# Kernel optimization log

Measured on AMD Instinct MI355X. Metric: run time of the kernel, lower is better.

Reference implementation:

```python
import jax, jax.numpy as jnp
import numpy as np


def setup_inputs() -> dict:
    key = jax.random.key(0)
    ks = jax.random.split(key, 9)
    N, K, CS, CT, OUT, S = 50000, 16, 64, 64, 64, 4
    x = jax.random.normal(ks[0], (N, CT), dtype=jnp.float32)
    src = jax.random.normal(ks[1], (N, CS), dtype=jnp.float32)
    neighbor_idx = jax.random.randint(ks[2], (N, K), 0, N, dtype=jnp.int32)
    scale_t = 1.0 / np.sqrt(CT)
    scale_s = 1.0 / np.sqrt(CS)
    Wt = jax.random.normal(ks[3], (CT, S), dtype=jnp.float32) * scale_t
    bt = jax.random.normal(ks[4], (S,), dtype=jnp.float32) * scale_t
    Ws = jax.random.normal(ks[5], (CS, S), dtype=jnp.float32) * scale_s
    bs = jax.random.normal(ks[6], (S,), dtype=jnp.float32) * scale_s
    W_lin = jax.random.normal(ks[7], (S, CS, OUT), dtype=jnp.float32) * scale_s
    b_lin = jax.random.normal(ks[8], (S, OUT), dtype=jnp.float32) * scale_s
    return {"x": x, "src": src, "neighbor_idx": neighbor_idx,
            "Wt": Wt, "bt": bt, "Ws": Ws, "bs": bs,
            "W_lin": W_lin, "b_lin": b_lin}


def reference(x, src, neighbor_idx, Wt, bt, Ws, bs, W_lin, b_lin):
    # Gather per-node neighbor messages: [N, K, Cs]
    msgs = src[neighbor_idx]
    size = Wt.shape[-1]
    # target assignment logits from own data: [N, S]
    t = x @ Wt + bt
    # source assignment logits from messages: [N, K, S]
    s = jnp.einsum('nkc,cs->nks', msgs, Ws) + bs
    # soft assignment over the `size` weight matrices (softmax over S)
    a = jax.nn.softmax(s + t[:, None, :], axis=-1)  # [N, K, S]
    # apply each of the `size` linears to the messages: [N, K, S, O]
    w = jnp.einsum('nkc,sco->nkso', msgs, W_lin) + b_lin
    # assignment-weighted mean over the S weight matrices: [N, K, O]
    out = jnp.einsum('nks,nkso->nko', a, w) / size
    return out
```

## Files before the change

kernel.cpp:

```cpp
#include <hip/hip_runtime.h>

#define CT 64
#define CS 64
#define K_NB 16
#define S_SZ 4
#define OUT_C 64
#define CAP 64

typedef float vfloat4 __attribute__((ext_vector_type(4)));

__global__ __launch_bounds__(256) void kt_rowlin(
    const float* __restrict__ in, const float* __restrict__ W,
    const float* __restrict__ b, float* __restrict__ outp, int N)
{
    int gt = blockIdx.x * 256 + threadIdx.x;
    int r = gt >> 3, part = gt & 7;
    if (r >= N) return;
    const float4* rv = (const float4*)(in + (size_t)r * 64) + part * 2;
    const float4* W4 = (const float4*)W;
    float4 q0 = rv[0], q1 = rv[1];
    int c0 = part * 8;
    float4 acc = {0.f, 0.f, 0.f, 0.f};
    float xc[8] = {q0.x, q0.y, q0.z, q0.w, q1.x, q1.y, q1.z, q1.w};
    #pragma unroll
    for (int u = 0; u < 8; ++u) {
        float4 wv = W4[c0 + u];
        acc.x = fmaf(xc[u], wv.x, acc.x);
        acc.y = fmaf(xc[u], wv.y, acc.y);
        acc.z = fmaf(xc[u], wv.z, acc.z);
        acc.w = fmaf(xc[u], wv.w, acc.w);
    }
    #pragma unroll
    for (int m = 1; m < 8; m <<= 1) {
        acc.x += __shfl_xor(acc.x, m);
        acc.y += __shfl_xor(acc.y, m);
        acc.z += __shfl_xor(acc.z, m);
        acc.w += __shfl_xor(acc.w, m);
    }
    if (part == 0) {
        float4 bb = *(const float4*)b;
        acc.x += bb.x; acc.y += bb.y; acc.z += bb.z; acc.w += bb.w;
        ((float4*)outp)[r] = acc;
    }
}

__global__ __launch_bounds__(256) void kh_zero(int* __restrict__ cursor, int N)
{
    int i = blockIdx.x * 256 + threadIdx.x;
    if (i < N) cursor[i] = 0;
}

__global__ __launch_bounds__(256) void kh_fill_fixed(
    const int* __restrict__ nidx, int* __restrict__ cursor,
    int* __restrict__ plist, int NK)
{
    int p = blockIdx.x * 256 + threadIdx.x;
    if (p >= NK) return;
    int j = nidx[p];
    int pos = atomicAdd(&cursor[j], 1);
    if (pos < CAP) plist[(size_t)j * CAP + pos] = p;
}

__global__ __launch_bounds__(256) void k_main(
    const int* __restrict__ cursor, const int* __restrict__ plist,
    const float* __restrict__ src,
    const float* __restrict__ W_lin, const float* __restrict__ b_lin,
    const float* __restrict__ t_in, const float* __restrict__ sl_in,
    float* __restrict__ out, int N)
{
    const int col = threadIdx.x;
    const int s = col >> 6, o = col & 63;
    float w[64];
    #pragma unroll
    for (int c = 0; c < 64; ++c)
        w[c] = W_lin[s * 4096 + (c << 6) + o];
    const float bl = b_lin[col];
    const int g = col >> 4;
    const int lane16 = col & 15;
    __shared__ float4 lsrc4[2][16];
    __shared__ float4 zl4[2][64];

    const int stride = gridDim.x;
    int j = blockIdx.x;
    int b = 0;
    if (j < N) {
        if (col < 16)
            lsrc4[0][col] = ((const float4*)(src + ((size_t)j << 6)))[col];
        __syncthreads();
    }
    for (; j < N; j += stride, b ^= 1) {
        const int jn = j + stride;
        {
            float a0 = bl, a1 = 0.f, a2 = 0.f, a3 = 0.f;
            #pragma unroll
            for (int c4 = 0; c4 < 16; ++c4) {
                float4 s4 = lsrc4[b][c4];
                a0 = fmaf(s4.x, w[c4 * 4 + 0], a0);
                a1 = fmaf(s4.y, w[c4 * 4 + 1], a1);
                a2 = fmaf(s4.z, w[c4 * 4 + 2], a2);
                a3 = fmaf(s4.w, w[c4 * 4 + 3], a3);
            }
            ((float*)zl4[b])[col] = (a0 + a1) + (a2 + a3);
        }
        if (jn < N && col < 16)
            lsrc4[b ^ 1][col] = ((const float4*)(src + ((size_t)jn << 6)))[col];
        const int cntr = cursor[j];
        const int cnt = cntr < CAP ? cntr : CAP;
        const float4 slv = ((const float4*)sl_in)[j];
        __syncthreads();
        const int off = j * CAP;
        for (int ib = g; ib < cnt; ib += 16) {
            const int p = plist[off + ib];
            const int n = p >> 4;
            float4 tv = ((const float4*)t_in)[n];
            float l0 = tv.x + slv.x, l1 = tv.y + slv.y;
            float l2 = tv.z + slv.z, l3 = tv.w + slv.w;
            float m = fmaxf(fmaxf(l0, l1), fmaxf(l2, l3));
            float e0 = __expf(l0 - m), e1 = __expf(l1 - m);
            float e2 = __expf(l2 - m), e3 = __expf(l3 - m);
            float inv = 0.25f / (e0 + e1 + e2 + e3);
            float4 z0 = zl4[b][lane16],      z1 = zl4[b][16 + lane16];
            float4 z2 = zl4[b][32 + lane16], z3 = zl4[b][48 + lane16];
            vfloat4 ov;
            ov.x = (e0 * z0.x + e1 * z1.x + e2 * z2.x + e3 * z3.x) * inv;
            ov.y = (e0 * z0.y + e1 * z1.y + e2 * z2.y + e3 * z3.y) * inv;
            ov.z = (e0 * z0.z + e1 * z1.z + e2 * z2.z + e3 * z3.z) * inv;
            ov.w = (e0 * z0.w + e1 * z1.w + e2 * z2.w + e3 * z3.w) * inv;
            __builtin_nontemporal_store(
                ov, (vfloat4*)out + (size_t)p * 16 + lane16);
        }
    }
}

extern "C" void kernel_launch(void* const* d_in, const int* in_sizes, int n_in,
                              void* d_out, int out_size, void* d_ws, size_t ws_size,
                              hipStream_t stream)
{
    const float* x   = (const float*)d_in[0];
    const float* src = (const float*)d_in[1];
    const int*   idx = (const int*)d_in[2];
    const float* Wt  = (const float*)d_in[3];
    const float* bt  = (const float*)d_in[4];
    const float* Ws  = (const float*)d_in[5];
    const float* bs  = (const float*)d_in[6];
    const float* Wl  = (const float*)d_in[7];
    const float* bl  = (const float*)d_in[8];
    float* out = (float*)d_out;

    const int N  = in_sizes[0] / CT;
    const int NK = N * K_NB;

    float* t  = (float*)d_ws;
    float* sl = t + (size_t)N * 4;
    int* cursor = (int*)(sl + (size_t)N * 4);
    int* plist  = cursor + N;

    const int gbN   = (N + 255) / 256;
    const int gbNK  = (NK + 255) / 256;
    const int gbRow = (N * 8 + 255) / 256;

    hipLaunchKernelGGL(kh_zero, dim3(gbN), dim3(256), 0, stream, cursor, N);
    hipLaunchKernelGGL(kh_fill_fixed, dim3(gbNK), dim3(256), 0, stream,
                       idx, cursor, plist, NK);
    hipLaunchKernelGGL(kt_rowlin, dim3(gbRow), dim3(256), 0, stream,
                       x, Wt, bt, t, N);
    hipLaunchKernelGGL(kt_rowlin, dim3(gbRow), dim3(256), 0, stream,
                       src, Ws, bs, sl, N);
    hipLaunchKernelGGL(k_main, dim3(2048), dim3(256), 0, stream,
                       cursor, plist, src, Wl, bl, t, sl, out, N);
}
```

Baseline: 385.6 us.

## Batch four source nodes per iteration in main kernel and fuse logit kernels

Merges the two row-linear logit kernels into one launch that computes both t and sl per row. The main scatter kernel now processes four source nodes per block iteration (JB=4), giving each barrier and each W_lin register load more work. Its grid changes from a fixed 2048 blocks to about N/16 blocks. Nontemporal loads are added for the neighbor index and plist reads. The larger batches bring more shared memory, more registers and an inner loop unrolled four times, and the grid size is now tied to N.

```diff
diff --git a/kernel.cpp b/kernel.cpp
--- a/kernel.cpp
+++ b/kernel.cpp
@@ -6,41 +6,57 @@
 #define S_SZ 4
 #define OUT_C 64
 #define CAP 64
+#define JB 4
 
 typedef float vfloat4 __attribute__((ext_vector_type(4)));
 
-__global__ __launch_bounds__(256) void kt_rowlin(
-    const float* __restrict__ in, const float* __restrict__ W,
-    const float* __restrict__ b, float* __restrict__ outp, int N)
+__global__ __launch_bounds__(256) void kt_both(
+    const float* __restrict__ x, const float* __restrict__ src,
+    const float* __restrict__ Wt, const float* __restrict__ bt,
+    const float* __restrict__ Ws, const float* __restrict__ bs,
+    float* __restrict__ t_out, float* __restrict__ sl_out, int N)
 {
     int gt = blockIdx.x * 256 + threadIdx.x;
     int r = gt >> 3, part = gt & 7;
     if (r >= N) return;
-    const float4* rv = (const float4*)(in + (size_t)r * 64) + part * 2;
-    const float4* W4 = (const float4*)W;
-    float4 q0 = rv[0], q1 = rv[1];
+    const float4* xv = (const float4*)(x   + (size_t)r * 64) + part * 2;
+    const float4* sv = (const float4*)(src + (size_t)r * 64) + part * 2;
+    const float4* Wt4 = (const float4*)Wt;
+    const float4* Ws4 = (const float4*)Ws;
+    float4 xq0 = xv[0], xq1 = xv[1];
+    float4 sq0 = sv[0], sq1 = sv[1];
     int c0 = part * 8;
-    float4 acc = {0.f, 0.f, 0.f, 0.f};
-    float xc[8] = {q0.x, q0.y, q0.z, q0.w, q1.x, q1.y, q1.z, q1.w};
+    float4 at = {0.f, 0.f, 0.f, 0.f};
+    float4 as = {0.f, 0.f, 0.f, 0.f};
+    float xc[8] = {xq0.x, xq0.y, xq0.z, xq0.w, xq1.x, xq1.y, xq1.z, xq1.w};
+    float sc[8] = {sq0.x, sq0.y, sq0.z, sq0.w, sq1.x, sq1.y, sq1.z, sq1.w};
     #pragma unroll
     for (int u = 0; u < 8; ++u) {
-        float4 wv = W4[c0 + u];
-        acc.x = fmaf(xc[u], wv.x, acc.x);
-        acc.y = fmaf(xc[u], wv.y, acc.y);
-        acc.z = fmaf(xc[u], wv.z, acc.z);
-        acc.w = fmaf(xc[u], wv.w, acc.w);
+        float4 wt = Wt4[c0 + u];
+        float4 ws = Ws4[c0 + u];
+        at.x = fmaf(xc[u], wt.x, at.x);
+        at.y = fmaf(xc[u], wt.y, at.y);
+        at.z = fmaf(xc[u], wt.z, at.z);
+        at.w = fmaf(xc[u], wt.w, at.w);
+        as.x = fmaf(sc[u], ws.x, as.x);
+        as.y = fmaf(sc[u], ws.y, as.y);
+        as.z = fmaf(sc[u], ws.z, as.z);
+        as.w = fmaf(sc[u], ws.w, as.w);
     }
     #pragma unroll
     for (int m = 1; m < 8; m <<= 1) {
-        acc.x += __shfl_xor(acc.x, m);
-        acc.y += __shfl_xor(acc.y, m);
-        acc.z += __shfl_xor(acc.z, m);
-        acc.w += __shfl_xor(acc.w, m);
+        at.x += __shfl_xor(at.x, m); at.y += __shfl_xor(at.y, m);
+        at.z += __shfl_xor(at.z, m); at.w += __shfl_xor(at.w, m);
+        as.x += __shfl_xor(as.x, m); as.y += __shfl_xor(as.y, m);
+        as.z += __shfl_xor(as.z, m); as.w += __shfl_xor(as.w, m);
     }
     if (part == 0) {
-        float4 bb = *(const float4*)b;
-        acc.x += bb.x; acc.y += bb.y; acc.z += bb.z; acc.w += bb.w;
-        ((float4*)outp)[r] = acc;
+        float4 bbt = *(const float4*)bt;
+        float4 bbs = *(const float4*)bs;
+        at.x += bbt.x; at.y += bbt.y; at.z += bbt.z; at.w += bbt.w;
+        as.x += bbs.x; as.y += bbs.y; as.z += bbs.z; as.w += bbs.w;
+        ((float4*)t_out)[r]  = at;
+        ((float4*)sl_out)[r] = as;
     }
 }
 
@@ -56,7 +72,7 @@
 {
     int p = blockIdx.x * 256 + threadIdx.x;
     if (p >= NK) return;
-    int j = nidx[p];
+    int j = __builtin_nontemporal_load(nidx + p);
     int pos = atomicAdd(&cursor[j], 1);
     if (pos < CAP) plist[(size_t)j * CAP + pos] = p;
 }
@@ -77,57 +93,84 @@
     const float bl = b_lin[col];
     const int g = col >> 4;
     const int lane16 = col & 15;
-    __shared__ float4 lsrc4[2][16];
-    __shared__ float4 zl4[2][64];
-
-    const int stride = gridDim.x;
-    int j = blockIdx.x;
+    __shared__ float4 lsrc4[2][JB][16];
+    __shared__ float4 zl4[2][JB][64];
+
+    const int pstride = gridDim.x * JB;
+    int jbase = blockIdx.x * JB;
     int b = 0;
-    if (j < N) {
-        if (col < 16)
-            lsrc4[0][col] = ((const float4*)(src + ((size_t)j << 6)))[col];
-        __syncthreads();
-    }
-    for (; j < N; j += stride, b ^= 1) {
-        const int jn = j + stride;
-        {
+    if (col < 16 * JB) {
+        int jj = col >> 4, q = col & 15;
+        int j0 = jbase + jj;
+        if (j0 < N)
+            lsrc4[0][jj][q] = ((const float4*)src)[((size_t)j0 << 4) + q];
+    }
+    __syncthreads();
+
+    for (; jbase < N; jbase += pstride, b ^= 1) {
+        #pragma unroll
+        for (int jj = 0; jj < JB; ++jj) {
             float a0 = bl, a1 = 0.f, a2 = 0.f, a3 = 0.f;
             #pragma unroll
             for (int c4 = 0; c4 < 16; ++c4) {
-                float4 s4 = lsrc4[b][c4];
+                float4 s4 = lsrc4[b][jj][c4];
                 a0 = fmaf(s4.x, w[c4 * 4 + 0], a0);
                 a1 = fmaf(s4.y, w[c4 * 4 + 1], a1);
                 a2 = fmaf(s4.z, w[c4 * 4 + 2], a2);
                 a3 = fmaf(s4.w, w[c4 * 4 + 3], a3);
             }
-            ((float*)zl4[b])[col] = (a0 + a1) + (a2 + a3);
-        }
-        if (jn < N && col < 16)
-            lsrc4[b ^ 1][col] = ((const float4*)(src + ((size_t)jn << 6)))[col];
-        const int cntr = cursor[j];
-        const int cnt = cntr < CAP ? cntr : CAP;
-        const float4 slv = ((const float4*)sl_in)[j];
+            ((float*)zl4[b][jj])[col] = (a0 + a1) + (a2 + a3);
+        }
+        {
+            int nb = jbase + pstride;
+            if (col < 16 * JB) {
+                int jj = col >> 4, q = col & 15;
+                int j0 = nb + jj;
+                if (j0 < N)
+                    lsrc4[b ^ 1][jj][q] =
+                        ((const float4*)src)[((size_t)j0 << 4) + q];
+            }
+        }
+        int cnt[JB]; float4 slv[JB];
+        #pragma unroll
+        for (int jj = 0; jj < JB; ++jj) {
+            int j = jbase + jj;
+            if (j < N) {
+                int c_ = cursor[j];
+                cnt[jj] = c_ < CAP ? c_ : CAP;
+                slv[jj] = ((const float4*)sl_in)[j];
+            } else {
+                cnt[jj] = 0;
+                slv[jj] = make_float4(0.f, 0.f, 0.f, 0.f);
+            }
+        }
         __syncthreads();
-        const int off = j * CAP;
-        for (int ib = g; ib < cnt; ib += 16) {
-            const int p = plist[off + ib];
-            const int n = p >> 4;
-            float4 tv = ((const float4*)t_in)[n];
-            float l0 = tv.x + slv.x, l1 = tv.y + slv.y;
-            float l2 = tv.z + slv.z, l3 = tv.w + slv.w;
-            float m = fmaxf(fmaxf(l0, l1), fmaxf(l2, l3));
-            float e0 = __expf(l0 - m), e1 = __expf(l1 - m);
-            float e2 = __expf(l2 - m), e3 = __expf(l3 - m);
-            float inv = 0.25f / (e0 + e1 + e2 + e3);
-            float4 z0 = zl4[b][lane16],      z1 = zl4[b][16 + lane16];
-            float4 z2 = zl4[b][32 + lane16], z3 = zl4[b][48 + lane16];
-            vfloat4 ov;
-            ov.x = (e0 * z0.x + e1 * z1.x + e2 * z2.x + e3 * z3.x) * inv;
-            ov.y = (e0 * z0.y + e1 * z1.y + e2 * z2.y + e3 * z3.y) * inv;
-            ov.z = (e0 * z0.z + e1 * z1.z + e2 * z2.z + e3 * z3.z) * inv;
-            ov.w = (e0 * z0.w + e1 * z1.w + e2 * z2.w + e3 * z3.w) * inv;
-            __builtin_nontemporal_store(
-                ov, (vfloat4*)out + (size_t)p * 16 + lane16);
+        #pragma unroll
+        for (int jj = 0; jj < JB; ++jj) {
+            const int off = (jbase + jj) * CAP;
+            const float4 sv = slv[jj];
+            for (int ib = g; ib < cnt[jj]; ib += 16) {
+                const int p = __builtin_nontemporal_load(plist + off + ib);
+                const int n = p >> 4;
+                float4 tv = ((const float4*)t_in)[n];
+                float l0 = tv.x + sv.x, l1 = tv.y + sv.y;
+                float l2 = tv.z + sv.z, l3 = tv.w + sv.w;
+                float m = fmaxf(fmaxf(l0, l1), fmaxf(l2, l3));
+                float e0 = __expf(l0 - m), e1 = __expf(l1 - m);
+                float e2 = __expf(l2 - m), e3 = __expf(l3 - m);
+                float inv = 0.25f / (e0 + e1 + e2 + e3);
+                float4 z0 = zl4[b][jj][lane16];
+                float4 z1 = zl4[b][jj][16 + lane16];
+                float4 z2 = zl4[b][jj][32 + lane16];
+                float4 z3 = zl4[b][jj][48 + lane16];
+                vfloat4 ov;
+                ov.x = (e0 * z0.x + e1 * z1.x + e2 * z2.x + e3 * z3.x) * inv;
+                ov.y = (e0 * z0.y + e1 * z1.y + e2 * z2.y + e3 * z3.y) * inv;
+                ov.z = (e0 * z0.z + e1 * z1.z + e2 * z2.z + e3 * z3.z) * inv;
+                ov.w = (e0 * z0.w + e1 * z1.w + e2 * z2.w + e3 * z3.w) * inv;
+                __builtin_nontemporal_store(
+                    ov, (vfloat4*)out + (size_t)p * 16 + lane16);
+            }
         }
     }
 }
@@ -158,14 +201,15 @@
     const int gbN   = (N + 255) / 256;
     const int gbNK  = (NK + 255) / 256;
     const int gbRow = (N * 8 + 255) / 256;
+    const int gbMain = (N + (256 * JB) - 1) / (256 * JB) * 256 / 256;
+    const int mainGrid = (N + JB * 4 - 1) / (JB * 4);
+    (void)gbMain;
 
     hipLaunchKernelGGL(kh_zero, dim3(gbN), dim3(256), 0, stream, cursor, N);
     hipLaunchKernelGGL(kh_fill_fixed, dim3(gbNK), dim3(256), 0, stream,
                        idx, cursor, plist, NK);
-    hipLaunchKernelGGL(kt_rowlin, dim3(gbRow), dim3(256), 0, stream,
-                       x, Wt, bt, t, N);
-    hipLaunchKernelGGL(kt_rowlin, dim3(gbRow), dim3(256), 0, stream,
-                       src, Ws, bs, sl, N);
-    hipLaunchKernelGGL(k_main, dim3(2048), dim3(256), 0, stream,
+    hipLaunchKernelGGL(kt_both, dim3(gbRow), dim3(256), 0, stream,
+                       x, src, Wt, bt, Ws, bs, t, sl, N);
+    hipLaunchKernelGGL(k_main, dim3(mainGrid), dim3(256), 0, stream,
                        cursor, plist, src, Wl, bl, t, sl, out, N);
 }
```

After: 379.5 us. About the same (-1.6%).
